# Performance work log

Measured on AMD Instinct MI355X. Metric: run time of the kernel, lower is better.

Reference implementation:

```python
import jax, jax.numpy as jnp
import numpy as np

EMBED_DIM = 1024
NUM_HEADS = 16
HEAD_DIM = EMBED_DIM // NUM_HEADS


def setup_inputs() -> dict:
    key = jax.random.key(0)
    k1, k2, k3, k4, k5 = jax.random.split(key, 5)
    x = jax.random.normal(k1, (4, 2048, EMBED_DIM), dtype=jnp.float32)
    # nn.Linear params: weight [out, in], bias [out]
    s_in = 1.0 / np.sqrt(EMBED_DIM)
    W_qkv = jax.random.uniform(k2, (3 * EMBED_DIM, EMBED_DIM), jnp.float32, -s_in, s_in)
    b_qkv = jax.random.uniform(k3, (3 * EMBED_DIM,), jnp.float32, -s_in, s_in)
    W_out = jax.random.uniform(k4, (EMBED_DIM, EMBED_DIM), jnp.float32, -s_in, s_in)
    b_out = jax.random.uniform(k5, (EMBED_DIM,), jnp.float32, -s_in, s_in)
    return {"x": x, "W_qkv": W_qkv, "b_qkv": b_qkv, "W_out": W_out, "b_out": b_out}


def reference(x, W_qkv, b_qkv, W_out, b_out):
    B, S, D = x.shape
    H, Dh = NUM_HEADS, HEAD_DIM
    qkv = x @ W_qkv.T + b_qkv                      # [B, S, 3D]
    qkv = qkv.reshape(B, S, 3, H, Dh)
    q = qkv[:, :, 0].transpose(0, 2, 1, 3)        # [B, H, S, Dh]
    k = qkv[:, :, 1].transpose(0, 2, 1, 3)
    v = qkv[:, :, 2].transpose(0, 2, 1, 3)
    scale = 1.0 / jnp.sqrt(jnp.asarray(Dh, x.dtype))
    scores = jnp.einsum('bhqd,bhkd->bhqk', q, k) * scale  # [B, H, S, S]
    attn = jax.nn.softmax(scores, axis=-1)
    out = jnp.einsum('bhqk,bhkd->bhqd', attn, v)  # [B, H, S, Dh]
    out = out.transpose(0, 2, 1, 3).reshape(B, S, D)
    return out @ W_out.T + b_out
```

## Files before the change

kernel.cpp:

```cpp
#include <hip/hip_runtime.h>

#define BB 4
#define SS 2048
#define DD 1024
#define HH 16
#define DHH 64
#define MM (BB*SS)

typedef __bf16 bf16x8 __attribute__((ext_vector_type(8)));
typedef __bf16 bf16x4 __attribute__((ext_vector_type(4)));
typedef float  f32x4  __attribute__((ext_vector_type(4)));

__device__ __forceinline__ unsigned short f2bf(float x) {
    unsigned int u = __float_as_uint(x);
    u += 0x7FFFu + ((u >> 16) & 1u);
    return (unsigned short)(u >> 16);
}

__device__ __forceinline__ void glds16(const __bf16* g, __bf16* l) {
    __builtin_amdgcn_global_load_lds(
        (const __attribute__((address_space(1))) void*)g,
        (__attribute__((address_space(3))) void*)l, 16, 0, 0);
}

__global__ __launch_bounds__(256) void cvt_all(
    const float4* __restrict__ x,  const float4* __restrict__ wq,
    const float4* __restrict__ wo,
    ushort4* __restrict__ xb, ushort4* __restrict__ wqb, ushort4* __restrict__ wob)
{
    int i = blockIdx.x * 256 + threadIdx.x;
    const float4* src; ushort4* dst; int j;
    if (i < 2097152)      { src = x;  dst = xb;  j = i; }
    else if (i < 2883584) { src = wq; dst = wqb; j = i - 2097152; }
    else                  { src = wo; dst = wob; j = i - 2883584; }
    float4 v = src[j];
    ushort4 o;
    o.x = f2bf(v.x); o.y = f2bf(v.y); o.z = f2bf(v.z); o.w = f2bf(v.w);
    dst[j] = o;
}

__global__ __launch_bounds__(256) void qkv_gemm(
    const __bf16* __restrict__ A,
    const __bf16* __restrict__ W,
    const float* __restrict__ bias,
    __bf16* __restrict__ Qp,
    __bf16* __restrict__ Kp,
    __bf16* __restrict__ Vp)
{
    __shared__ __bf16 smem[16896];
#define CT(r,c) smem[(r)*132 + (c)]
    __bf16* As = smem;
    __bf16* Bs = smem + 8192;
    const int tid  = threadIdx.x;
    const int m0   = blockIdx.x * 128;
    const int n0   = blockIdx.y * 128;
    const int lane = tid & 63;
    const int wid  = tid >> 6;
    const int fr   = lane & 15;
    const int quad = lane >> 4;
    const int wm   = (wid >> 1) * 64;
    const int wn   = (wid & 1) * 64;

    const int srow = lane >> 3;
    const int sg   = ((lane & 7) - srow) & 7;

    f32x4 acc[4][4] = {};

    for (int k0 = 0; k0 < DD; k0 += 64) {
        __syncthreads();
        #pragma unroll
        for (int p = 0; p < 4; ++p) {
            int cidx = p * 4 + wid;
            int r = cidx * 8 + srow;
            glds16(A + (size_t)(m0 + r) * DD + k0 + sg * 8, As + cidx * 512);
            glds16(W + (size_t)(n0 + r) * DD + k0 + sg * 8, Bs + cidx * 512);
        }
        __syncthreads();

        bf16x8 af[2][4], bw[2][4];
        #pragma unroll
        for (int kc = 0; kc < 2; ++kc)
            #pragma unroll
            for (int t = 0; t < 4; ++t) {
                int col = ((kc * 4 + quad + fr) & 7) * 8;
                af[kc][t] = *(const bf16x8*)&As[(wm + t*16 + fr) * 64 + col];
                bw[kc][t] = *(const bf16x8*)&Bs[(wn + t*16 + fr) * 64 + col];
            }
        #pragma unroll
        for (int kc = 0; kc < 2; ++kc)
            #pragma unroll
            for (int mt = 0; mt < 4; ++mt)
                #pragma unroll
                for (int nt = 0; nt < 4; ++nt)
                    acc[mt][nt] = __builtin_amdgcn_mfma_f32_16x16x32_bf16(
                        af[kc][mt], bw[kc][nt], acc[mt][nt], 0, 0, 0);
    }

    __syncthreads();
    const int t3 = n0 >> 10;
    const int b  = m0 >> 11;
    const int s0 = m0 & (SS - 1);

    float bn[4];
    #pragma unroll
    for (int nt = 0; nt < 4; ++nt) bn[nt] = bias[n0 + wn + nt*16 + fr];

    if (t3 == 2) {
        #pragma unroll
        for (int nt = 0; nt < 4; ++nt)
            #pragma unroll
            for (int mt = 0; mt < 4; ++mt) {
                f32x4 t;
                #pragma unroll
                for (int i = 0; i < 4; ++i) t[i] = acc[mt][nt][i] + bn[nt];
                *(bf16x4*)&CT(wn + nt*16 + fr, wm + mt*16 + quad*4) =
                    __builtin_convertvector(t, bf16x4);
            }
        __syncthreads();
        const int pn0 = n0 - 2048;
        #pragma unroll
        for (int p = 0; p < 8; ++p) {
            int g = tid + p * 256;
            int r = g >> 4;
            int c = (g & 15) << 3;
            int pn = pn0 + r, h = pn >> 6, dh = pn & 63;
            *(uint4*)&Vp[((size_t)((b*HH + h)*DHH + dh))*SS + s0 + c] = *(uint4*)&CT(r, c);
        }
    } else {
        __bf16* dst = (t3 == 0) ? Qp : Kp;
        const float qscale = (t3 == 0) ? 0.125f * 1.44269504088896340736f : 1.0f;
        #pragma unroll
        for (int nt = 0; nt < 4; ++nt)
            #pragma unroll
            for (int mt = 0; mt < 4; ++mt)
                #pragma unroll
                for (int i = 0; i < 4; ++i)
                    CT(wm + mt*16 + quad*4 + i, wn + nt*16 + fr) =
                        (__bf16)((acc[mt][nt][i] + bn[nt]) * qscale);
        __syncthreads();
        const int pn0 = (t3 == 0) ? n0 : n0 - 1024;
        #pragma unroll
        for (int p = 0; p < 8; ++p) {
            int g = tid + p * 256;
            int r = g >> 4;
            int c = (g & 15) << 3;
            int pn = pn0 + c, h = pn >> 6, dh = pn & 63;
            *(uint4*)&dst[((size_t)((b*HH + h))*SS + s0 + r)*DHH + dh] = *(uint4*)&CT(r, c);
        }
    }
#undef CT
}

__global__ __launch_bounds__(256) void out_gemm(
    const __bf16* __restrict__ A,
    const __bf16* __restrict__ W,
    const float* __restrict__ bias,
    float* __restrict__ out)
{
    __shared__ __bf16 smem[16384];
    __bf16* As = smem;
    __bf16* Bs = smem + 8192;
    const int tid  = threadIdx.x;
    const int m0   = blockIdx.x * 128;
    const int n0   = blockIdx.y * 128;
    const int lane = tid & 63;
    const int wid  = tid >> 6;
    const int fr   = lane & 15;
    const int quad = lane >> 4;
    const int wm   = (wid >> 1) * 64;
    const int wn   = (wid & 1) * 64;

    const int srow = lane >> 3;
    const int sg   = ((lane & 7) - srow) & 7;

    f32x4 acc[4][4] = {};

    for (int k0 = 0; k0 < DD; k0 += 64) {
        __syncthreads();
        #pragma unroll
        for (int p = 0; p < 4; ++p) {
            int cidx = p * 4 + wid;
            int r = cidx * 8 + srow;
            glds16(A + (size_t)(m0 + r) * DD + k0 + sg * 8, As + cidx * 512);
            glds16(W + (size_t)(n0 + r) * DD + k0 + sg * 8, Bs + cidx * 512);
        }
        __syncthreads();

        bf16x8 af[2][4], bw[2][4];
        #pragma unroll
        for (int kc = 0; kc < 2; ++kc)
            #pragma unroll
            for (int t = 0; t < 4; ++t) {
                int col = ((kc * 4 + quad + fr) & 7) * 8;
                af[kc][t] = *(const bf16x8*)&As[(wm + t*16 + fr) * 64 + col];
                bw[kc][t] = *(const bf16x8*)&Bs[(wn + t*16 + fr) * 64 + col];
            }
        #pragma unroll
        for (int kc = 0; kc < 2; ++kc)
            #pragma unroll
            for (int mt = 0; mt < 4; ++mt)
                #pragma unroll
                for (int nt = 0; nt < 4; ++nt)
                    acc[mt][nt] = __builtin_amdgcn_mfma_f32_16x16x32_bf16(
                        af[kc][mt], bw[kc][nt], acc[mt][nt], 0, 0, 0);
    }

    #pragma unroll
    for (int nt = 0; nt < 4; ++nt) {
        int n  = n0 + wn + nt*16 + fr;
        float bnv = bias[n];
        #pragma unroll
        for (int mt = 0; mt < 4; ++mt) {
            #pragma unroll
            for (int i = 0; i < 4; ++i) {
                int m = m0 + wm + mt*16 + quad*4 + i;
                out[(size_t)m * DD + n] = acc[mt][nt][i] + bnv;
            }
        }
    }
}

__global__ __launch_bounds__(256, 2) void attn_mfma(
    const __bf16* __restrict__ Qp,
    const __bf16* __restrict__ Kp,
    const __bf16* __restrict__ Vp,
    __bf16* __restrict__ Op)
{
    __shared__ __bf16 Ks[2][64 * 64];
    __shared__ __bf16 VT[2][64 * 64];
    __shared__ __bf16 Ps[256][72];
    __shared__ float  Ls[256];

    const int tid  = threadIdx.x;
    const int q0   = blockIdx.x * 256;
    const int bh   = blockIdx.y;
    const size_t base = (size_t)bh * SS * DHH;
    const int lane = tid & 63;
    const int wid  = tid >> 6;
    const int fr   = lane & 15;
    const int quad = lane >> 4;
    const int wrow = wid * 64;

    const int srow = lane >> 3;
    const int sg   = ((lane & 7) - srow) & 7;

#define STAGE_KV(buf, kt_)                                                        \
    {                                                                             \
        _Pragma("unroll")                                                         \
        for (int p = 0; p < 2; ++p) {                                             \
            int cidx = p * 4 + wid;                  \
            int r = cidx * 8 + srow;                                              \
            glds16(Kp + base + (size_t)((kt_) + r) * DHH + sg * 8,                \
                   &Ks[buf][cidx * 512]);                                         \
            glds16(Vp + base + (size_t)r * SS + (kt_) + sg * 8,                   \
                   &VT[buf][cidx * 512]);                                         \
        }                                                                         \
    }

    bf16x8 aq[4][2];
    #pragma unroll
    for (int nt = 0; nt < 4; ++nt)
        #pragma unroll
        for (int kc = 0; kc < 2; ++kc)
            aq[nt][kc] = *(const bf16x8*)
                (Qp + base + (size_t)(q0 + wrow + nt*16 + fr) * DHH + kc*32 + quad*8);

    f32x4 o[4][4] = {};
    float lp[4] = {};

    STAGE_KV(0, 0)
    __syncthreads();

    int cur = 0;
    for (int kt = 0; kt < SS; kt += 64) {
        if (kt + 64 < SS) STAGE_KV(cur ^ 1, kt + 64)
        const __bf16* Kc = Ks[cur];
        const __bf16* Vc = VT[cur];

        #pragma unroll
        for (int mt = 0; mt < 4; ++mt) {
            bf16x8 bk[2];
            #pragma unroll
            for (int kc = 0; kc < 2; ++kc)
                bk[kc] = *(const bf16x8*)
                    &Kc[(mt*16 + fr) * 64 + ((kc*4 + quad + fr) & 7) * 8];
            f32x4 s[4] = {};
            __builtin_amdgcn_s_setprio(1);
            #pragma unroll
            for (int nt = 0; nt < 4; ++nt)
                #pragma unroll
                for (int kc = 0; kc < 2; ++kc)
                    s[nt] = __builtin_amdgcn_mfma_f32_16x16x32_bf16(
                        bk[kc], aq[nt][kc], s[nt], 0, 0, 0);
            __builtin_amdgcn_s_setprio(0);
            #pragma unroll
            for (int nt = 0; nt < 4; ++nt) {
                f32x4 ev;
                ev[0] = __builtin_amdgcn_exp2f(s[nt][0]);
                ev[1] = __builtin_amdgcn_exp2f(s[nt][1]);
                ev[2] = __builtin_amdgcn_exp2f(s[nt][2]);
                ev[3] = __builtin_amdgcn_exp2f(s[nt][3]);
                lp[nt] += (ev[0] + ev[1]) + (ev[2] + ev[3]);
                *(bf16x4*)&Ps[wrow + nt*16 + fr][mt*16 + quad*4] =
                    __builtin_convertvector(ev, bf16x4);
            }
        }

        #pragma unroll
        for (int mt = 0; mt < 4; ++mt) {
            bf16x8 ap[2];
            #pragma unroll
            for (int kc = 0; kc < 2; ++kc)
                ap[kc] = *(const bf16x8*)&Ps[wrow + mt*16 + fr][kc*32 + quad*8];
            __builtin_amdgcn_s_setprio(1);
            #pragma unroll
            for (int nt = 0; nt < 4; ++nt)
                #pragma unroll
                for (int kc = 0; kc < 2; ++kc) {
                    bf16x8 bv = *(const bf16x8*)
                        &Vc[(nt*16 + fr) * 64 + ((kc*4 + quad + fr) & 7) * 8];
                    o[mt][nt] = __builtin_amdgcn_mfma_f32_16x16x32_bf16(
                        ap[kc], bv, o[mt][nt], 0, 0, 0);
                }
            __builtin_amdgcn_s_setprio(0);
        }

        __syncthreads();
        cur ^= 1;
    }
#undef STAGE_KV

    #pragma unroll
    for (int nt = 0; nt < 4; ++nt) {
        float v = lp[nt];
        v += __shfl_xor(v, 16);
        v += __shfl_xor(v, 32);
        Ls[wrow + nt*16 + fr] = v;
    }

    #pragma unroll
    for (int mt = 0; mt < 4; ++mt)
        #pragma unroll
        for (int i = 0; i < 4; ++i) {
            float inv = 1.0f / Ls[wrow + mt*16 + quad*4 + i];
            #pragma unroll
            for (int nt = 0; nt < 4; ++nt)
                Ps[wrow + mt*16 + quad*4 + i][nt*16 + fr] = (__bf16)(o[mt][nt][i] * inv);
        }
    __syncthreads();

    const int b = bh >> 4, h = bh & (HH - 1);
    #pragma unroll
    for (int p = 0; p < 8; ++p) {
        int g = tid + p * 256;
        int r = g >> 3;
        int c = (g & 7) << 3;
        *(uint4*)&Op[((size_t)(b*SS + q0 + r))*DD + h*DHH + c] = *(uint4*)&Ps[r][c];
    }
}


extern "C" void kernel_launch(void* const* d_in, const int* in_sizes, int n_in,
                              void* d_out, int out_size, void* d_ws, size_t ws_size,
                              hipStream_t stream)
{
    const float* x     = (const float*)d_in[0];
    const float* W_qkv = (const float*)d_in[1];
    const float* b_qkv = (const float*)d_in[2];
    const float* W_out = (const float*)d_in[3];
    const float* b_out = (const float*)d_in[4];
    float* out = (float*)d_out;

    __bf16* ws  = (__bf16*)d_ws;
    __bf16* xb  = ws;
    __bf16* wqb = xb  + (size_t)8388608;
    __bf16* wob = wqb + (size_t)3145728;
    __bf16* qp  = wob + (size_t)1048576;
    __bf16* kp  = qp  + (size_t)8388608;
    __bf16* vp  = kp  + (size_t)8388608;
    __bf16* op  = vp  + (size_t)8388608;

    cvt_all<<<12288, 256, 0, stream>>>(
        (const float4*)x, (const float4*)W_qkv, (const float4*)W_out,
        (ushort4*)xb, (ushort4*)wqb, (ushort4*)wob);

    qkv_gemm<<<dim3(MM/128, 3*DD/128), 256, 0, stream>>>(xb, wqb, b_qkv, qp, kp, vp);
    attn_mfma<<<dim3(SS/256, BB*HH), 256, 0, stream>>>(qp, kp, vp, op);
    out_gemm<<<dim3(MM/128, DD/128), 256, 0, stream>>>(op, wob, b_out, out);
}
```

Baseline: 265.6 us.

## Switch attention to 32x32x16 MFMA and keep P in registers via permlane swaps

Rewrites the attention inner loop to use 32x32x16 bf16 MFMA tiles instead of 16x16x32. The softmax probabilities are packed with v_cvt_pk_bf16_f32 and redistributed across lanes with v_permlane32_swap, so they feed the PV MFMA straight from registers rather than round-tripping through the LDS Ps buffer. The aim is to cut LDS traffic and per-tile instruction overhead. In exchange it relies on exact MFMA lane layouts and raises register pressure from holding the packed P words.

```diff
diff --git a/kernel.cpp b/kernel.cpp
--- a/kernel.cpp
+++ b/kernel.cpp
@@ -10,6 +10,9 @@
 typedef __bf16 bf16x8 __attribute__((ext_vector_type(8)));
 typedef __bf16 bf16x4 __attribute__((ext_vector_type(4)));
 typedef float  f32x4  __attribute__((ext_vector_type(4)));
+typedef float  f32x16 __attribute__((ext_vector_type(16)));
+typedef unsigned int u32;
+typedef unsigned int u32x4 __attribute__((ext_vector_type(4)));
 
 __device__ __forceinline__ unsigned short f2bf(float x) {
     unsigned int u = __float_as_uint(x);
@@ -237,8 +240,8 @@
     const size_t base = (size_t)bh * SS * DHH;
     const int lane = tid & 63;
     const int wid  = tid >> 6;
-    const int fr   = lane & 15;
-    const int quad = lane >> 4;
+    const int c32  = lane & 31;
+    const int hi   = lane >> 5;
     const int wrow = wid * 64;
 
     const int srow = lane >> 3;
@@ -257,16 +260,16 @@
         }                                                                         \
     }
 
-    bf16x8 aq[4][2];
-    #pragma unroll
-    for (int nt = 0; nt < 4; ++nt)
-        #pragma unroll
-        for (int kc = 0; kc < 2; ++kc)
-            aq[nt][kc] = *(const bf16x8*)
-                (Qp + base + (size_t)(q0 + wrow + nt*16 + fr) * DHH + kc*32 + quad*8);
-
-    f32x4 o[4][4] = {};
-    float lp[4] = {};
+    bf16x8 bq[2][4];
+    #pragma unroll
+    for (int qt = 0; qt < 2; ++qt)
+        #pragma unroll
+        for (int ks = 0; ks < 4; ++ks)
+            bq[qt][ks] = *(const bf16x8*)
+                (Qp + base + (size_t)(q0 + wrow + qt*32 + c32) * DHH + ks*16 + hi*8);
+
+    f32x16 o[2][2] = {};
+    float lp[2] = {};
 
     STAGE_KV(0, 0)
     __syncthreads();
@@ -277,52 +280,65 @@
         const __bf16* Kc = Ks[cur];
         const __bf16* Vc = VT[cur];
 
-        #pragma unroll
-        for (int mt = 0; mt < 4; ++mt) {
-            bf16x8 bk[2];
-            #pragma unroll
-            for (int kc = 0; kc < 2; ++kc)
-                bk[kc] = *(const bf16x8*)
-                    &Kc[(mt*16 + fr) * 64 + ((kc*4 + quad + fr) & 7) * 8];
-            f32x4 s[4] = {};
+        u32 pw[2][2][8];
+
+        #pragma unroll
+        for (int kt2 = 0; kt2 < 2; ++kt2) {
+            bf16x8 bk[4];
+            #pragma unroll
+            for (int ks = 0; ks < 4; ++ks)
+                bk[ks] = *(const bf16x8*)
+                    &Kc[(kt2*32 + c32) * 64 + ((ks*2 + hi + c32) & 7) * 8];
+            #pragma unroll
+            for (int qt = 0; qt < 2; ++qt) {
+                f32x16 s = {};
+                __builtin_amdgcn_s_setprio(1);
+                #pragma unroll
+                for (int ks = 0; ks < 4; ++ks)
+                    s = __builtin_amdgcn_mfma_f32_32x32x16_bf16(
+                        bk[ks], bq[qt][ks], s, 0, 0, 0);
+                __builtin_amdgcn_s_setprio(0);
+                #pragma unroll
+                for (int e = 0; e < 16; ++e) s[e] = __builtin_amdgcn_exp2f(s[e]);
+                lp[qt] += ((s[0]+s[1])+(s[2]+s[3])) + ((s[4]+s[5])+(s[6]+s[7]))
+                        + ((s[8]+s[9])+(s[10]+s[11])) + ((s[12]+s[13])+(s[14]+s[15]));
+                #pragma unroll
+                for (int kk = 0; kk < 2; ++kk) {
+                    u32 wa, wb, wc, wd;
+                    asm("v_cvt_pk_bf16_f32 %0, %1, %2" : "=v"(wa) : "v"(s[kk*8+0]), "v"(s[kk*8+1]));
+                    asm("v_cvt_pk_bf16_f32 %0, %1, %2" : "=v"(wb) : "v"(s[kk*8+4]), "v"(s[kk*8+5]));
+                    asm("v_cvt_pk_bf16_f32 %0, %1, %2" : "=v"(wc) : "v"(s[kk*8+2]), "v"(s[kk*8+3]));
+                    asm("v_cvt_pk_bf16_f32 %0, %1, %2" : "=v"(wd) : "v"(s[kk*8+6]), "v"(s[kk*8+7]));
+                    asm("v_permlane32_swap_b32 %0, %1" : "+v"(wa), "+v"(wb));
+                    asm("v_permlane32_swap_b32 %0, %1" : "+v"(wc), "+v"(wd));
+                    pw[qt][kt2][kk*4+0] = wa;
+                    pw[qt][kt2][kk*4+1] = wc;
+                    pw[qt][kt2][kk*4+2] = wb;
+                    pw[qt][kt2][kk*4+3] = wd;
+                }
+            }
+        }
+
+        #pragma unroll
+        for (int ks = 0; ks < 4; ++ks) {
+            const int kt2 = ks >> 1, kk = ks & 1;
+            bf16x8 bv[2];
+            #pragma unroll
+            for (int dt = 0; dt < 2; ++dt)
+                bv[dt] = *(const bf16x8*)
+                    &Vc[(dt*32 + c32) * 64 + ((ks*2 + hi + c32) & 7) * 8];
             __builtin_amdgcn_s_setprio(1);
             #pragma unroll
-            for (int nt = 0; nt < 4; ++nt)
-                #pragma unroll
-                for (int kc = 0; kc < 2; ++kc)
-                    s[nt] = __builtin_amdgcn_mfma_f32_16x16x32_bf16(
-                        bk[kc], aq[nt][kc], s[nt], 0, 0, 0);
+            for (int qt = 0; qt < 2; ++qt) {
+                u32x4 t = { pw[qt][kt2][kk*4+0], pw[qt][kt2][kk*4+1],
+                            pw[qt][kt2][kk*4+2], pw[qt][kt2][kk*4+3] };
+                bf16x8 pa = __builtin_bit_cast(bf16x8, t);
+                #pragma unroll
+                for (int dt = 0; dt < 2; ++dt)
+                    o[qt][dt] = __builtin_amdgcn_mfma_f32_32x32x16_bf16(
+                        pa, bv[dt], o[qt][dt], 0, 0, 0);
+            }
             __builtin_amdgcn_s_setprio(0);
-            #pragma unroll
-            for (int nt = 0; nt < 4; ++nt) {
-                f32x4 ev;
-                ev[0] = __builtin_amdgcn_exp2f(s[nt][0]);
-                ev[1] = __builtin_amdgcn_exp2f(s[nt][1]);
-                ev[2] = __builtin_amdgcn_exp2f(s[nt][2]);
-                ev[3] = __builtin_amdgcn_exp2f(s[nt][3]);
-                lp[nt] += (ev[0] + ev[1]) + (ev[2] + ev[3]);
-                *(bf16x4*)&Ps[wrow + nt*16 + fr][mt*16 + quad*4] =
-                    __builtin_convertvector(ev, bf16x4);
-            }
-        }
-
-        #pragma unroll
-        for (int mt = 0; mt < 4; ++mt) {
-            bf16x8 ap[2];
-            #pragma unroll
-            for (int kc = 0; kc < 2; ++kc)
-                ap[kc] = *(const bf16x8*)&Ps[wrow + mt*16 + fr][kc*32 + quad*8];
-            __builtin_amdgcn_s_setprio(1);
-            #pragma unroll
-            for (int nt = 0; nt < 4; ++nt)
-                #pragma unroll
-                for (int kc = 0; kc < 2; ++kc) {
-                    bf16x8 bv = *(const bf16x8*)
-                        &Vc[(nt*16 + fr) * 64 + ((kc*4 + quad + fr) & 7) * 8];
-                    o[mt][nt] = __builtin_amdgcn_mfma_f32_16x16x32_bf16(
-                        ap[kc], bv, o[mt][nt], 0, 0, 0);
-                }
-            __builtin_amdgcn_s_setprio(0);
         }
 
         __syncthreads();
@@ -331,21 +347,20 @@
 #undef STAGE_KV
 
     #pragma unroll
-    for (int nt = 0; nt < 4; ++nt) {
-        float v = lp[nt];
-        v += __shfl_xor(v, 16);
-        v += __shfl_xor(v, 32);
-        Ls[wrow + nt*16 + fr] = v;
-    }
-
-    #pragma unroll
-    for (int mt = 0; mt < 4; ++mt)
-        #pragma unroll
-        for (int i = 0; i < 4; ++i) {
-            float inv = 1.0f / Ls[wrow + mt*16 + quad*4 + i];
-            #pragma unroll
-            for (int nt = 0; nt < 4; ++nt)
-                Ps[wrow + mt*16 + quad*4 + i][nt*16 + fr] = (__bf16)(o[mt][nt][i] * inv);
+    for (int qt = 0; qt < 2; ++qt) {
+        float v = lp[qt] + __shfl_xor(lp[qt], 32);
+        Ls[wrow + qt*32 + c32] = v;
+    }
+
+    #pragma unroll
+    for (int qt = 0; qt < 2; ++qt)
+        #pragma unroll
+        for (int r = 0; r < 16; ++r) {
+            int row = wrow + qt*32 + (r & 3) + 8*(r >> 2) + 4*hi;
+            float inv = 1.0f / Ls[row];
+            #pragma unroll
+            for (int dt = 0; dt < 2; ++dt)
+                Ps[row][dt*32 + c32] = (__bf16)(o[qt][dt][r] * inv);
         }
     __syncthreads();
 
```

Result: no change. 264.1 us (-0.6%).
